# Optimization experiments

Hardware: AMD Instinct MI355X
Metric: run time of the kernel (lower is better)

The kernel has to match this reference:

```python
import jax, jax.numpy as jnp
import numpy as np

N_NODES = 50000
N_EDGES = 800000
H_DIM = 64
N_RELS = 8
N_BASES = 2
N_LAYERS = 2


def setup_inputs() -> dict:
    key = jax.random.key(0)
    ks = jax.random.split(key, 10)
    scale = 1.0 / np.sqrt(H_DIM)
    features = jax.random.normal(ks[0], (N_NODES, H_DIM), dtype=jnp.float32)
    src = jax.random.randint(ks[1], (N_EDGES,), 0, N_NODES, dtype=jnp.int32)
    dst = jax.random.randint(ks[2], (N_EDGES,), 0, N_NODES, dtype=jnp.int32)
    etype = jax.random.randint(ks[3], (N_EDGES,), 0, N_RELS, dtype=jnp.int32)
    # basis weights V: [L, B, H, H], coefficients comp: [L, R, B]
    V = jax.random.normal(ks[4], (N_LAYERS, N_BASES, H_DIM, H_DIM), dtype=jnp.float32) * scale
    comp = jax.random.normal(ks[5], (N_LAYERS, N_RELS, N_BASES), dtype=jnp.float32)
    loop_w = jax.random.normal(ks[6], (N_LAYERS, H_DIM, H_DIM), dtype=jnp.float32) * scale
    layer_bias = jnp.zeros((N_LAYERS, H_DIM), dtype=jnp.float32)
    fc_w = jax.random.normal(ks[7], (1, N_NODES * H_DIM), dtype=jnp.float32) * (1.0 / np.sqrt(N_NODES * H_DIM))
    fc_b = jnp.zeros((1,), dtype=jnp.float32)
    return {
        "features": features, "V": V, "comp": comp, "loop_w": loop_w,
        "layer_bias": layer_bias, "fc_w": fc_w, "fc_b": fc_b,
        "src": src, "dst": dst, "etype": etype,
    }


def reference(features, V, comp, loop_w, layer_bias, fc_w, fc_b, src, dst, etype):
    N, H = features.shape
    L = V.shape[0]
    x = features
    for l in range(L):
        # basis decomposition: project nodes through each basis first (N*B*H, cheap),
        # then mix per-edge with relation coefficients -> avoids per-edge [H,H] weights
        proj = jnp.einsum('ni,bio->nbo', x, V[l])          # [N, B, H]
        msg = jnp.einsum('eb,ebo->eo', comp[l][etype], proj[src])  # [E, H]
        agg = jax.ops.segment_sum(msg, dst, num_segments=N)        # [N, H]
        h = agg + x @ loop_w[l] + layer_bias[l]
        x = jax.nn.relu(h) if l < L - 1 else h
    flat = x.reshape(1, -1)                                # [1, N*H]
    return jax.nn.sigmoid(flat @ fc_w.T + fc_b)            # [1, 1]
```

## Files before the change

kernel.cpp:

```cpp
#include <hip/hip_runtime.h>
#include <hip/hip_bf16.h>
#include <math.h>

#define N_NODES 50000
#define N_EDGES 800000
#define HDIM 64

#define NBUCKET 392
#define BSHIFT  7
#define NLOC    128
#define BCAP    3072

typedef short bf16x8 __attribute__((ext_vector_type(8)));
typedef float f32x4  __attribute__((ext_vector_type(4)));
typedef unsigned short ushort_t;

__device__ __forceinline__ ushort_t f2bf(float f) {
    __hip_bfloat16 b = __float2bfloat16(f);
    return *(ushort_t*)&b;
}

__global__ __launch_bounds__(256) void prep_kernel(
    const float* __restrict__ features, ushort_t* __restrict__ x_bf,
    const float* __restrict__ V, const float* __restrict__ lw,
    ushort_t* __restrict__ Wt, int* __restrict__ bucketFill,
    float* __restrict__ scalar, int* __restrict__ done)
{
    const int b = blockIdx.x;
    const int t = threadIdx.x;
    if (b < 3125) {
        const int i = b * 256 + t;
        const float4 v = ((const float4*)features)[i];
        ushort4 o = { f2bf(v.x), f2bf(v.y), f2bf(v.z), f2bf(v.w) };
        *(ushort4*)&x_bf[(size_t)i * 4] = o;
    } else if (b < 3221) {
        const int e = (b - 3125) * 256 + t;
        const int l = e / 12288, r = e % 12288;
        const int n = r / 192, k = r % 192;
        const int sel = k >> 6, i = k & 63;
        const float val = (sel < 2) ? V[l * 8192 + sel * 4096 + i * 64 + n]
                                    : lw[l * 4096 + i * 64 + n];
        Wt[e] = f2bf(val);
    } else {
        for (int i = t; i < NBUCKET; i += 256) bucketFill[i] = 0;
        if (t == 0) { scalar[0] = 0.0f; done[0] = 0; }
    }
}

__global__ __launch_bounds__(256) void bucket_scatter(
    const int* __restrict__ src, const int* __restrict__ dst,
    const int* __restrict__ etype, int* __restrict__ bucketFill,
    unsigned int* __restrict__ buf)
{
    __shared__ int cnt[NBUCKET];
    __shared__ int base[NBUCKET];
    const int t = threadIdx.x;
    for (int i = t; i < NBUCKET; i += 256) cnt[i] = 0;
    __syncthreads();

    int rank[8], bkt[8];
    unsigned pay[8];
    bool valid[8];
#pragma unroll
    for (int k = 0; k < 8; ++k) {
        const int e = blockIdx.x * 2048 + k * 256 + t;
        valid[k] = (e < N_EDGES);
        if (valid[k]) {
            const int d = dst[e];
            const int b = d >> BSHIFT;
            bkt[k] = b;
            pay[k] = (unsigned)src[e] | ((unsigned)etype[e] << 16)
                   | ((unsigned)(d & (NLOC - 1)) << 19);
            rank[k] = atomicAdd(&cnt[b], 1);
        }
    }
    __syncthreads();
    for (int i = t; i < NBUCKET; i += 256)
        base[i] = atomicAdd(&bucketFill[i], cnt[i]);
    __syncthreads();
#pragma unroll
    for (int k = 0; k < 8; ++k) {
        if (valid[k]) {
            const int pos = base[bkt[k]] + rank[k];
            if (pos < BCAP) buf[bkt[k] * BCAP + pos] = pay[k];
        }
    }
}

__global__ __launch_bounds__(256) void bucket_sort(
    const unsigned int* __restrict__ buf, const int* __restrict__ bucketFill,
    unsigned int* __restrict__ edges, int* __restrict__ row_ptr)
{
    __shared__ int hist[NLOC];
    __shared__ int lscan[NLOC];
    __shared__ int cnt2[NLOC];
    __shared__ int sraw[448];
    __shared__ int sexc[448];
    const int b = blockIdx.x;
    const int t = threadIdx.x;

    if (t < NLOC) { hist[t] = 0; cnt2[t] = 0; }
    for (int i = t; i < 448; i += 256)
        sraw[i] = (i < NBUCKET) ? bucketFill[i] : 0;
    __syncthreads();

    if (t < 64) {
        int carry = 0;
        for (int c = 0; c < 7; ++c) {
            const int h = sraw[c * 64 + t];
            int x = h;
#pragma unroll
            for (int off = 1; off < 64; off <<= 1) {
                int u = __shfl_up(x, off, 64);
                if (t >= off) x += u;
            }
            sexc[c * 64 + t] = carry + x - h;
            carry += __shfl(x, 63, 64);
        }
    }
    __syncthreads();
    const int cntb = min(sraw[b], BCAP);
    const int bb   = sexc[b];

    for (int i0 = t; i0 < cntb; i0 += 1024) {
        const bool v1 = i0 + 256 < cntb, v2 = i0 + 512 < cntb, v3 = i0 + 768 < cntb;
        const unsigned p0 = buf[b * BCAP + i0];
        unsigned p1 = 0, p2 = 0, p3 = 0;
        if (v1) p1 = buf[b * BCAP + i0 + 256];
        if (v2) p2 = buf[b * BCAP + i0 + 512];
        if (v3) p3 = buf[b * BCAP + i0 + 768];
        atomicAdd(&hist[p0 >> 19], 1);
        if (v1) atomicAdd(&hist[p1 >> 19], 1);
        if (v2) atomicAdd(&hist[p2 >> 19], 1);
        if (v3) atomicAdd(&hist[p3 >> 19], 1);
    }
    __syncthreads();

    if (t < 64) {
        int carry = 0;
        for (int c = 0; c < 2; ++c) {
            const int h = hist[c * 64 + t];
            int x = h;
#pragma unroll
            for (int off = 1; off < 64; off <<= 1) {
                int u = __shfl_up(x, off, 64);
                if (t >= off) x += u;
            }
            lscan[c * 64 + t] = carry + x - h;
            carry += __shfl(x, 63, 64);
        }
    }
    __syncthreads();

    const int n0 = b << BSHIFT;
    if (t < NLOC) {
        const int g = n0 + t;
        if (g < N_NODES) row_ptr[g] = bb + lscan[t];
    }
    if (b == NBUCKET - 1 && t == 0) row_ptr[N_NODES] = bb + cntb;

    for (int i0 = t; i0 < cntb; i0 += 1024) {
        const bool v1 = i0 + 256 < cntb, v2 = i0 + 512 < cntb, v3 = i0 + 768 < cntb;
        const unsigned p0 = buf[b * BCAP + i0];
        unsigned p1 = 0, p2 = 0, p3 = 0;
        if (v1) p1 = buf[b * BCAP + i0 + 256];
        if (v2) p2 = buf[b * BCAP + i0 + 512];
        if (v3) p3 = buf[b * BCAP + i0 + 768];
        {
            const int d = p0 >> 19;
            const int r = atomicAdd(&cnt2[d], 1);
            edges[bb + lscan[d] + r] = p0;
        }
        if (v1) { const int d = p1 >> 19; const int r = atomicAdd(&cnt2[d], 1);
                  edges[bb + lscan[d] + r] = p1; }
        if (v2) { const int d = p2 >> 19; const int r = atomicAdd(&cnt2[d], 1);
                  edges[bb + lscan[d] + r] = p2; }
        if (v3) { const int d = p3 >> 19; const int r = atomicAdd(&cnt2[d], 1);
                  edges[bb + lscan[d] + r] = p3; }
    }
}

__global__ __launch_bounds__(256) void aggregate_v4(
    const ushort_t* __restrict__ x,
    const unsigned int* __restrict__ edges,
    const int* __restrict__ row_ptr,
    const float* __restrict__ comp_l,
    ushort_t* __restrict__ y)
{
    __shared__ float scomp[16];
    const int t = threadIdx.x;
    if (t < 16) scomp[t] = comp_l[t];
    __syncthreads();

    const int lane = t & 63;
    const int wv   = t >> 6;
    const int g    = lane >> 4;
    const int fq   = lane & 15;
    const int n    = blockIdx.x * 16 + wv * 4 + g;

    const int beg = row_ptr[n];
    const int end = row_ptr[n + 1];

    float a0[4], a1[4];
#pragma unroll
    for (int i = 0; i < 4; ++i) { a0[i] = 0.f; a1[i] = 0.f; }

    for (int j = beg; j < end; j += 4) {
        unsigned p[4];
#pragma unroll
        for (int k = 0; k < 4; ++k) {
            const int e = j + k;
            p[k] = edges[(e < end) ? e : (end - 1)];
        }
        uint2 u[4];
#pragma unroll
        for (int k = 0; k < 4; ++k)
            u[k] = *(const uint2*)&x[(size_t)(p[k] & 0xFFFFu) * 64 + fq * 4];
        float2 c[4];
#pragma unroll
        for (int k = 0; k < 4; ++k) {
            c[k] = *(const float2*)&scomp[((p[k] >> 16) & 7u) * 2];
            if (j + k >= end) { c[k].x = 0.f; c[k].y = 0.f; }
        }
#pragma unroll
        for (int k = 0; k < 4; ++k) {
            const float f0 = __uint_as_float(u[k].x << 16);
            const float f1 = __uint_as_float(u[k].x & 0xFFFF0000u);
            const float f2 = __uint_as_float(u[k].y << 16);
            const float f3 = __uint_as_float(u[k].y & 0xFFFF0000u);
            a0[0] = fmaf(c[k].x, f0, a0[0]); a1[0] = fmaf(c[k].y, f0, a1[0]);
            a0[1] = fmaf(c[k].x, f1, a0[1]); a1[1] = fmaf(c[k].y, f1, a1[1]);
            a0[2] = fmaf(c[k].x, f2, a0[2]); a1[2] = fmaf(c[k].y, f2, a1[2]);
            a0[3] = fmaf(c[k].x, f3, a0[3]); a1[3] = fmaf(c[k].y, f3, a1[3]);
        }
    }

    ushort4 s0 = { f2bf(a0[0]), f2bf(a0[1]), f2bf(a0[2]), f2bf(a0[3]) };
    ushort4 s1 = { f2bf(a1[0]), f2bf(a1[1]), f2bf(a1[2]), f2bf(a1[3]) };
    *(ushort4*)&y[(size_t)n * 128 + fq * 4]      = s0;
    *(ushort4*)&y[(size_t)n * 128 + 64 + fq * 4] = s1;
}

template <bool FUSE>
__global__ __launch_bounds__(256) void mfma_transform(
    const ushort_t* __restrict__ y_bf,
    const ushort_t* __restrict__ x_bf,
    const ushort_t* __restrict__ Wt,
    const float* __restrict__ bias,
    const float* __restrict__ fcw,
    ushort_t* __restrict__ xout,
    float* __restrict__ scalar,
    const float* __restrict__ fcb,
    int* __restrict__ done,
    float* __restrict__ outp)
{
    __shared__ __align__(16) ushort_t su[64 * 200];
    __shared__ float sred[4];
    const int t = threadIdx.x;
    const int w = t >> 6;
    const int lane = t & 63;
    const int c16 = lane & 15;
    const int quad = lane >> 4;
    const int tile = blockIdx.x;

    bf16x8 wf[6];
#pragma unroll
    for (int kf = 0; kf < 6; ++kf)
        wf[kf] = *(const bf16x8*)&Wt[(w * 16 + c16) * 192 + kf * 32 + quad * 8];
    const float bv = bias[w * 16 + c16];

#pragma unroll
    for (int k = 0; k < 6; ++k) {
        const int cid = t + 256 * k;
        const int row = cid / 24;
        const int part = cid % 24;
        const int n = tile * 64 + row;
        uint4 v = {0u, 0u, 0u, 0u};
        if (n < N_NODES) {
            v = (part < 16) ? *(const uint4*)&y_bf[(size_t)n * 128 + part * 8]
                            : *(const uint4*)&x_bf[(size_t)n * 64 + (part - 16) * 8];
        }
        *(uint4*)&su[row * 200 + part * 8] = v;
    }
    __syncthreads();

    float fsum = 0.f;
#pragma unroll
    for (int mt = 0; mt < 4; ++mt) {
        f32x4 acc = {bv, bv, bv, bv};
#pragma unroll
        for (int kf = 0; kf < 6; ++kf) {
            const bf16x8 af =
                *(const bf16x8*)&su[(mt * 16 + c16) * 200 + kf * 32 + quad * 8];
            acc = __builtin_amdgcn_mfma_f32_16x16x32_bf16(af, wf[kf], acc, 0, 0, 0);
        }
        const int nodeb = tile * 64 + mt * 16 + quad * 4;
        if (FUSE) {
#pragma unroll
            for (int r = 0; r < 4; ++r) {
                const int n = nodeb + r;
                if (n < N_NODES)
                    fsum += acc[r] * fcw[(size_t)n * 64 + w * 16 + c16];
            }
        } else {
#pragma unroll
            for (int r = 0; r < 4; ++r) {
                const int n = nodeb + r;
                if (n < N_NODES)
                    xout[(size_t)n * 64 + w * 16 + c16] = f2bf(fmaxf(acc[r], 0.f));
            }
        }
    }

    if (FUSE) {
#pragma unroll
        for (int off = 32; off; off >>= 1) fsum += __shfl_down(fsum, off, 64);
        if (lane == 0) sred[w] = fsum;
        __syncthreads();
        if (t == 0) {
            atomicAdd(scalar, sred[0] + sred[1] + sred[2] + sred[3]);
            __threadfence();
            const int ticket = atomicAdd(done, 1);
            if (ticket == (int)gridDim.x - 1) {
                const float v = atomicAdd(scalar, 0.0f) + fcb[0];
                outp[0] = 1.0f / (1.0f + expf(-v));
            }
        }
    }
}

extern "C" void kernel_launch(void* const* d_in, const int* in_sizes, int n_in,
                              void* d_out, int out_size, void* d_ws, size_t ws_size,
                              hipStream_t stream)
{
    const float* features = (const float*)d_in[0];
    const float* V        = (const float*)d_in[1];
    const float* comp     = (const float*)d_in[2];
    const float* loop_w   = (const float*)d_in[3];
    const float* bias     = (const float*)d_in[4];
    const float* fc_w     = (const float*)d_in[5];
    const float* fc_b     = (const float*)d_in[6];
    const int*   src      = (const int*)d_in[7];
    const int*   dst      = (const int*)d_in[8];
    const int*   etype    = (const int*)d_in[9];
    float* out = (float*)d_out;

    char* ws = (char*)d_ws;
    ushort_t*     y_bf    = (ushort_t*)(ws);
    ushort_t*     x_bf    = (ushort_t*)(ws + 12800000);
    ushort_t*     x1_bf   = (ushort_t*)(ws + 19200000);
    ushort_t*     Wt      = (ushort_t*)(ws + 25600000);
    float*        scalar  = (float*)   (ws + 25649152);
    int*          done    = (int*)     (ws + 25649156);
    int*          bucketFill = (int*)  (ws + 25649280);
    int*          row_ptr = (int*)     (ws + 25650944);
    unsigned int* edges   = (unsigned int*)(ws + 25851008);
    unsigned int* buf     = (unsigned int*)(ws + 29051008);

    const int aggBlocks = N_NODES / 16;
    const int mtBlocks  = (N_NODES + 63) / 64;
    const int k1Blocks  = (N_EDGES + 2047) / 2048;

    prep_kernel<<<3222, 256, 0, stream>>>(features, x_bf, V, loop_w, Wt,
                                          bucketFill, scalar, done);
    bucket_scatter<<<k1Blocks, 256, 0, stream>>>(src, dst, etype, bucketFill, buf);
    bucket_sort<<<NBUCKET, 256, 0, stream>>>(buf, bucketFill, edges, row_ptr);

    aggregate_v4<<<aggBlocks, 256, 0, stream>>>(x_bf, edges, row_ptr, comp, y_bf);
    mfma_transform<false><<<mtBlocks, 256, 0, stream>>>(
        y_bf, x_bf, Wt, bias, nullptr, x1_bf, nullptr, nullptr, nullptr, nullptr);

    aggregate_v4<<<aggBlocks, 256, 0, stream>>>(x1_bf, edges, row_ptr, comp + 16, y_bf);
    mfma_transform<true><<<mtBlocks, 256, 0, stream>>>(
        y_bf, x1_bf, Wt + 12288, bias + 64, fc_w, nullptr, scalar, fc_b, done, out);
}
```

Measured before the change: 188.8 us.

## Gather FP8 node features in aggregation and fuse prep with edge bucketing

Node features are also written as FP8 e4m3 copies, which the aggregation kernels gather instead of bf16, halving the bytes per random row gather. Edge indices are now prefetched one iteration ahead in the aggregation loop. The prep and bucket-scatter kernels are merged into one launch, and the counter zeroing moves to a memset. The cost is extra FP8 writes and lower precision in the aggregated messages, which could matter for accuracy.

```diff
diff --git a/kernel.cpp b/kernel.cpp
--- a/kernel.cpp
+++ b/kernel.cpp
@@ -1,5 +1,6 @@
 #include <hip/hip_runtime.h>
 #include <hip/hip_bf16.h>
+#include <hip/hip_fp8.h>
 #include <math.h>
 
 #define N_NODES 50000
@@ -14,26 +15,69 @@
 typedef short bf16x8 __attribute__((ext_vector_type(8)));
 typedef float f32x4  __attribute__((ext_vector_type(4)));
 typedef unsigned short ushort_t;
+typedef unsigned char uchar_t;
 
 __device__ __forceinline__ ushort_t f2bf(float f) {
     __hip_bfloat16 b = __float2bfloat16(f);
     return *(ushort_t*)&b;
 }
 
-__global__ __launch_bounds__(256) void prep_kernel(
+__device__ __forceinline__ unsigned pk_fp8x4(float a, float b, float c, float d) {
+#if __has_builtin(__builtin_amdgcn_cvt_pk_fp8_f32)
+    int r = __builtin_amdgcn_cvt_pk_fp8_f32(a, b, 0, false);
+    r = __builtin_amdgcn_cvt_pk_fp8_f32(c, d, r, true);
+    return (unsigned)r;
+#else
+    __hip_fp8_e4m3 fa(a), fb(b), fc(c), fd(d);
+    return (unsigned)fa.__x | ((unsigned)fb.__x << 8)
+         | ((unsigned)fc.__x << 16) | ((unsigned)fd.__x << 24);
+#endif
+}
+__device__ __forceinline__ uchar_t f2fp8(float a) {
+#if __has_builtin(__builtin_amdgcn_cvt_pk_fp8_f32)
+    return (uchar_t)(__builtin_amdgcn_cvt_pk_fp8_f32(a, 0.f, 0, false) & 0xFF);
+#else
+    __hip_fp8_e4m3 fa(a);
+    return (uchar_t)fa.__x;
+#endif
+}
+__device__ __forceinline__ void fp8x4_to_f32(unsigned u, float* f) {
+#if __has_builtin(__builtin_amdgcn_cvt_f32_fp8)
+    f[0] = __builtin_amdgcn_cvt_f32_fp8(u, 0);
+    f[1] = __builtin_amdgcn_cvt_f32_fp8(u, 1);
+    f[2] = __builtin_amdgcn_cvt_f32_fp8(u, 2);
+    f[3] = __builtin_amdgcn_cvt_f32_fp8(u, 3);
+#else
+    __hip_fp8_e4m3 v0, v1, v2, v3;
+    v0.__x = (uchar_t)(u);       v1.__x = (uchar_t)(u >> 8);
+    v2.__x = (uchar_t)(u >> 16); v3.__x = (uchar_t)(u >> 24);
+    f[0] = (float)v0; f[1] = (float)v1; f[2] = (float)v2; f[3] = (float)v3;
+#endif
+}
+
+__global__ __launch_bounds__(256) void prep_scatter(
     const float* __restrict__ features, ushort_t* __restrict__ x_bf,
+    uchar_t* __restrict__ x8,
     const float* __restrict__ V, const float* __restrict__ lw,
-    ushort_t* __restrict__ Wt, int* __restrict__ bucketFill,
-    float* __restrict__ scalar, int* __restrict__ done)
+    ushort_t* __restrict__ Wt,
+    const int* __restrict__ src, const int* __restrict__ dst,
+    const int* __restrict__ etype, int* __restrict__ bucketFill,
+    unsigned int* __restrict__ buf)
 {
+    __shared__ int cnt[NBUCKET];
+    __shared__ int base[NBUCKET];
     const int b = blockIdx.x;
     const int t = threadIdx.x;
+
     if (b < 3125) {
         const int i = b * 256 + t;
         const float4 v = ((const float4*)features)[i];
         ushort4 o = { f2bf(v.x), f2bf(v.y), f2bf(v.z), f2bf(v.w) };
         *(ushort4*)&x_bf[(size_t)i * 4] = o;
-    } else if (b < 3221) {
+        ((unsigned*)x8)[i] = pk_fp8x4(v.x, v.y, v.z, v.w);
+        return;
+    }
+    if (b < 3221) {
         const int e = (b - 3125) * 256 + t;
         const int l = e / 12288, r = e % 12288;
         const int n = r / 192, k = r % 192;
@@ -41,20 +85,10 @@
         const float val = (sel < 2) ? V[l * 8192 + sel * 4096 + i * 64 + n]
                                     : lw[l * 4096 + i * 64 + n];
         Wt[e] = f2bf(val);
-    } else {
-        for (int i = t; i < NBUCKET; i += 256) bucketFill[i] = 0;
-        if (t == 0) { scalar[0] = 0.0f; done[0] = 0; }
-    }
-}
-
-__global__ __launch_bounds__(256) void bucket_scatter(
-    const int* __restrict__ src, const int* __restrict__ dst,
-    const int* __restrict__ etype, int* __restrict__ bucketFill,
-    unsigned int* __restrict__ buf)
-{
-    __shared__ int cnt[NBUCKET];
-    __shared__ int base[NBUCKET];
-    const int t = threadIdx.x;
+        return;
+    }
+
+    const int sb = b - 3221;
     for (int i = t; i < NBUCKET; i += 256) cnt[i] = 0;
     __syncthreads();
 
@@ -63,15 +97,15 @@
     bool valid[8];
 #pragma unroll
     for (int k = 0; k < 8; ++k) {
-        const int e = blockIdx.x * 2048 + k * 256 + t;
+        const int e = sb * 2048 + k * 256 + t;
         valid[k] = (e < N_EDGES);
         if (valid[k]) {
             const int d = dst[e];
-            const int b = d >> BSHIFT;
-            bkt[k] = b;
+            const int bk = d >> BSHIFT;
+            bkt[k] = bk;
             pay[k] = (unsigned)src[e] | ((unsigned)etype[e] << 16)
                    | ((unsigned)(d & (NLOC - 1)) << 19);
-            rank[k] = atomicAdd(&cnt[b], 1);
+            rank[k] = atomicAdd(&cnt[bk], 1);
         }
     }
     __syncthreads();
@@ -180,8 +214,8 @@
     }
 }
 
-__global__ __launch_bounds__(256) void aggregate_v4(
-    const ushort_t* __restrict__ x,
+__global__ __launch_bounds__(256) void aggregate_v6(
+    const uchar_t* __restrict__ x8,
     const unsigned int* __restrict__ edges,
     const int* __restrict__ row_ptr,
     const float* __restrict__ comp_l,
@@ -205,33 +239,36 @@
 #pragma unroll
     for (int i = 0; i < 4; ++i) { a0[i] = 0.f; a1[i] = 0.f; }
 
-    for (int j = beg; j < end; j += 4) {
-        unsigned p[4];
-#pragma unroll
-        for (int k = 0; k < 4; ++k) {
-            const int e = j + k;
-            p[k] = edges[(e < end) ? e : (end - 1)];
-        }
-        uint2 u[4];
-#pragma unroll
-        for (int k = 0; k < 4; ++k)
-            u[k] = *(const uint2*)&x[(size_t)(p[k] & 0xFFFFu) * 64 + fq * 4];
-        float2 c[4];
-#pragma unroll
-        for (int k = 0; k < 4; ++k) {
-            c[k] = *(const float2*)&scomp[((p[k] >> 16) & 7u) * 2];
-            if (j + k >= end) { c[k].x = 0.f; c[k].y = 0.f; }
-        }
-#pragma unroll
-        for (int k = 0; k < 4; ++k) {
-            const float f0 = __uint_as_float(u[k].x << 16);
-            const float f1 = __uint_as_float(u[k].x & 0xFFFF0000u);
-            const float f2 = __uint_as_float(u[k].y << 16);
-            const float f3 = __uint_as_float(u[k].y & 0xFFFF0000u);
-            a0[0] = fmaf(c[k].x, f0, a0[0]); a1[0] = fmaf(c[k].y, f0, a1[0]);
-            a0[1] = fmaf(c[k].x, f1, a0[1]); a1[1] = fmaf(c[k].y, f1, a1[1]);
-            a0[2] = fmaf(c[k].x, f2, a0[2]); a1[2] = fmaf(c[k].y, f2, a1[2]);
-            a0[3] = fmaf(c[k].x, f3, a0[3]); a1[3] = fmaf(c[k].y, f3, a1[3]);
+    if (beg < end) {
+        unsigned pc[4];
+#pragma unroll
+        for (int k = 0; k < 4; ++k) pc[k] = edges[min(beg + k, end - 1)];
+
+        for (int j = beg; j < end; j += 4) {
+            unsigned u[4];
+#pragma unroll
+            for (int k = 0; k < 4; ++k)
+                u[k] = *(const unsigned*)&x8[(size_t)(pc[k] & 0xFFFFu) * 64 + fq * 4];
+            unsigned pn[4];
+#pragma unroll
+            for (int k = 0; k < 4; ++k) pn[k] = edges[min(j + 4 + k, end - 1)];
+            float2 c[4];
+#pragma unroll
+            for (int k = 0; k < 4; ++k) {
+                c[k] = *(const float2*)&scomp[((pc[k] >> 16) & 7u) * 2];
+                if (j + k >= end) { c[k].x = 0.f; c[k].y = 0.f; }
+            }
+#pragma unroll
+            for (int k = 0; k < 4; ++k) {
+                float f[4];
+                fp8x4_to_f32(u[k], f);
+                a0[0] = fmaf(c[k].x, f[0], a0[0]); a1[0] = fmaf(c[k].y, f[0], a1[0]);
+                a0[1] = fmaf(c[k].x, f[1], a0[1]); a1[1] = fmaf(c[k].y, f[1], a1[1]);
+                a0[2] = fmaf(c[k].x, f[2], a0[2]); a1[2] = fmaf(c[k].y, f[2], a1[2]);
+                a0[3] = fmaf(c[k].x, f[3], a0[3]); a1[3] = fmaf(c[k].y, f[3], a1[3]);
+            }
+#pragma unroll
+            for (int k = 0; k < 4; ++k) pc[k] = pn[k];
         }
     }
 
@@ -249,6 +286,7 @@
     const float* __restrict__ bias,
     const float* __restrict__ fcw,
     ushort_t* __restrict__ xout,
+    uchar_t* __restrict__ xout8,
     float* __restrict__ scalar,
     const float* __restrict__ fcb,
     int* __restrict__ done,
@@ -306,8 +344,11 @@
 #pragma unroll
             for (int r = 0; r < 4; ++r) {
                 const int n = nodeb + r;
-                if (n < N_NODES)
-                    xout[(size_t)n * 64 + w * 16 + c16] = f2bf(fmaxf(acc[r], 0.f));
+                if (n < N_NODES) {
+                    const float rl = fmaxf(acc[r], 0.f);
+                    xout[(size_t)n * 64 + w * 16 + c16]  = f2bf(rl);
+                    xout8[(size_t)n * 64 + w * 16 + c16] = f2fp8(rl);
+                }
             }
         }
     }
@@ -349,28 +390,31 @@
     ushort_t*     y_bf    = (ushort_t*)(ws);
     ushort_t*     x_bf    = (ushort_t*)(ws + 12800000);
     ushort_t*     x1_bf   = (ushort_t*)(ws + 19200000);
-    ushort_t*     Wt      = (ushort_t*)(ws + 25600000);
-    float*        scalar  = (float*)   (ws + 25649152);
-    int*          done    = (int*)     (ws + 25649156);
-    int*          bucketFill = (int*)  (ws + 25649280);
-    int*          row_ptr = (int*)     (ws + 25650944);
-    unsigned int* edges   = (unsigned int*)(ws + 25851008);
-    unsigned int* buf     = (unsigned int*)(ws + 29051008);
+    uchar_t*      x8      = (uchar_t*) (ws + 25600000);
+    uchar_t*      x1_8    = (uchar_t*) (ws + 28800000);
+    ushort_t*     Wt      = (ushort_t*)(ws + 32000000);
+    float*        scalar  = (float*)   (ws + 32049152);
+    int*          done    = (int*)     (ws + 32049156);
+    int*          bucketFill = (int*)  (ws + 32049160);
+    int*          row_ptr = (int*)     (ws + 32051072);
+    unsigned int* edges   = (unsigned int*)(ws + 32251264);
+    unsigned int* buf     = (unsigned int*)(ws + 35451264);
 
     const int aggBlocks = N_NODES / 16;
     const int mtBlocks  = (N_NODES + 63) / 64;
-    const int k1Blocks  = (N_EDGES + 2047) / 2048;
-
-    prep_kernel<<<3222, 256, 0, stream>>>(features, x_bf, V, loop_w, Wt,
-                                          bucketFill, scalar, done);
-    bucket_scatter<<<k1Blocks, 256, 0, stream>>>(src, dst, etype, bucketFill, buf);
+    const int psBlocks  = 3221 + 391;
+
+    hipMemsetAsync(scalar, 0, 1576, stream);
+    prep_scatter<<<psBlocks, 256, 0, stream>>>(features, x_bf, x8, V, loop_w, Wt,
+                                               src, dst, etype, bucketFill, buf);
     bucket_sort<<<NBUCKET, 256, 0, stream>>>(buf, bucketFill, edges, row_ptr);
 
-    aggregate_v4<<<aggBlocks, 256, 0, stream>>>(x_bf, edges, row_ptr, comp, y_bf);
+    aggregate_v6<<<aggBlocks, 256, 0, stream>>>(x8, edges, row_ptr, comp, y_bf);
     mfma_transform<false><<<mtBlocks, 256, 0, stream>>>(
-        y_bf, x_bf, Wt, bias, nullptr, x1_bf, nullptr, nullptr, nullptr, nullptr);
-
-    aggregate_v4<<<aggBlocks, 256, 0, stream>>>(x1_bf, edges, row_ptr, comp + 16, y_bf);
+        y_bf, x_bf, Wt, bias, nullptr, x1_bf, x1_8, nullptr, nullptr, nullptr, nullptr);
+
+    aggregate_v6<<<aggBlocks, 256, 0, stream>>>(x1_8, edges, row_ptr, comp + 16, y_bf);
     mfma_transform<true><<<mtBlocks, 256, 0, stream>>>(
-        y_bf, x1_bf, Wt + 12288, bias + 64, fc_w, nullptr, scalar, fc_b, done, out);
-}
+        y_bf, x1_bf, Wt + 12288, bias + 64, fc_w, nullptr, nullptr,
+        scalar, fc_b, done, out);
+}
```

New measurement: 193.4 us. 2.4% more time.

## Sort nodes by degree within buckets to balance aggregation wavefronts

Applied to the files above, without the earlier changes.

The bucket sort now also counting-sorts the 128 nodes of each bucket by in-degree and writes a permutation array. The aggregation kernel walks nodes in that order, so the four nodes sharing a wavefront have similar edge counts and less time is lost to divergent loop trip counts. Padding slots beyond N_NODES are skipped. The cost is an extra indirection load per node, scattered output writes, and a small amount of extra work in the sort kernel.

```diff
diff --git a/kernel.cpp b/kernel.cpp
--- a/kernel.cpp
+++ b/kernel.cpp
@@ -10,6 +10,7 @@
 #define BSHIFT  7
 #define NLOC    128
 #define BCAP    3072
+#define NVIRT   (NBUCKET * NLOC)
 
 typedef short bf16x8 __attribute__((ext_vector_type(8)));
 typedef float f32x4  __attribute__((ext_vector_type(4)));
@@ -89,13 +90,15 @@
 
 __global__ __launch_bounds__(256) void bucket_sort(
     const unsigned int* __restrict__ buf, const int* __restrict__ bucketFill,
-    unsigned int* __restrict__ edges, int* __restrict__ row_ptr)
+    unsigned int* __restrict__ edges, int* __restrict__ row_ptr,
+    int* __restrict__ perm)
 {
     __shared__ int hist[NLOC];
     __shared__ int lscan[NLOC];
     __shared__ int cnt2[NLOC];
     __shared__ int sraw[448];
     __shared__ int sexc[448];
+    __shared__ int dh[64];
     const int b = blockIdx.x;
     const int t = threadIdx.x;
 
@@ -159,6 +162,27 @@
     }
     if (b == NBUCKET - 1 && t == 0) row_ptr[N_NODES] = bb + cntb;
 
+    if (t < 64) dh[t] = 0;
+    __syncthreads();
+    if (t < NLOC) atomicAdd(&dh[min(hist[t], 63)], 1);
+    __syncthreads();
+    if (t < 64) {
+        const int h = dh[t];
+        int x = h;
+#pragma unroll
+        for (int off = 1; off < 64; off <<= 1) {
+            int u = __shfl_up(x, off, 64);
+            if (t >= off) x += u;
+        }
+        dh[t] = x - h;
+    }
+    __syncthreads();
+    if (t < NLOC) {
+        const int dr  = min(hist[t], 63);
+        const int pos = atomicAdd(&dh[dr], 1);
+        perm[n0 + pos] = n0 + t;
+    }
+
     for (int i0 = t; i0 < cntb; i0 += 1024) {
         const bool v1 = i0 + 256 < cntb, v2 = i0 + 512 < cntb, v3 = i0 + 768 < cntb;
         const unsigned p0 = buf[b * BCAP + i0];
@@ -180,10 +204,11 @@
     }
 }
 
-__global__ __launch_bounds__(256) void aggregate_v4(
+__global__ __launch_bounds__(256) void aggregate_v7(
     const ushort_t* __restrict__ x,
     const unsigned int* __restrict__ edges,
     const int* __restrict__ row_ptr,
+    const int* __restrict__ perm,
     const float* __restrict__ comp_l,
     ushort_t* __restrict__ y)
 {
@@ -196,10 +221,11 @@
     const int wv   = t >> 6;
     const int g    = lane >> 4;
     const int fq   = lane & 15;
-    const int n    = blockIdx.x * 16 + wv * 4 + g;
-
-    const int beg = row_ptr[n];
-    const int end = row_ptr[n + 1];
+    const int vi   = blockIdx.x * 16 + wv * 4 + g;
+    const int n    = perm[vi];
+
+    int beg = 0, end = 0;
+    if (n < N_NODES) { beg = row_ptr[n]; end = row_ptr[n + 1]; }
 
     float a0[4], a1[4];
 #pragma unroll
@@ -235,10 +261,12 @@
         }
     }
 
-    ushort4 s0 = { f2bf(a0[0]), f2bf(a0[1]), f2bf(a0[2]), f2bf(a0[3]) };
-    ushort4 s1 = { f2bf(a1[0]), f2bf(a1[1]), f2bf(a1[2]), f2bf(a1[3]) };
-    *(ushort4*)&y[(size_t)n * 128 + fq * 4]      = s0;
-    *(ushort4*)&y[(size_t)n * 128 + 64 + fq * 4] = s1;
+    if (n < N_NODES) {
+        ushort4 s0 = { f2bf(a0[0]), f2bf(a0[1]), f2bf(a0[2]), f2bf(a0[3]) };
+        ushort4 s1 = { f2bf(a1[0]), f2bf(a1[1]), f2bf(a1[2]), f2bf(a1[3]) };
+        *(ushort4*)&y[(size_t)n * 128 + fq * 4]      = s0;
+        *(ushort4*)&y[(size_t)n * 128 + 64 + fq * 4] = s1;
+    }
 }
 
 template <bool FUSE>
@@ -356,21 +384,24 @@
     int*          row_ptr = (int*)     (ws + 25650944);
     unsigned int* edges   = (unsigned int*)(ws + 25851008);
     unsigned int* buf     = (unsigned int*)(ws + 29051008);
-
-    const int aggBlocks = N_NODES / 16;
+    int*          perm    = (int*)     (ws + 33867904);
+
+    const int aggBlocks = NVIRT / 16;
     const int mtBlocks  = (N_NODES + 63) / 64;
     const int k1Blocks  = (N_EDGES + 2047) / 2048;
 
     prep_kernel<<<3222, 256, 0, stream>>>(features, x_bf, V, loop_w, Wt,
                                           bucketFill, scalar, done);
     bucket_scatter<<<k1Blocks, 256, 0, stream>>>(src, dst, etype, bucketFill, buf);
-    bucket_sort<<<NBUCKET, 256, 0, stream>>>(buf, bucketFill, edges, row_ptr);
-
-    aggregate_v4<<<aggBlocks, 256, 0, stream>>>(x_bf, edges, row_ptr, comp, y_bf);
+    bucket_sort<<<NBUCKET, 256, 0, stream>>>(buf, bucketFill, edges, row_ptr, perm);
+
+    aggregate_v7<<<aggBlocks, 256, 0, stream>>>(x_bf, edges, row_ptr, perm,
+                                                comp, y_bf);
     mfma_transform<false><<<mtBlocks, 256, 0, stream>>>(
         y_bf, x_bf, Wt, bias, nullptr, x1_bf, nullptr, nullptr, nullptr, nullptr);
 
-    aggregate_v4<<<aggBlocks, 256, 0, stream>>>(x1_bf, edges, row_ptr, comp + 16, y_bf);
+    aggregate_v7<<<aggBlocks, 256, 0, stream>>>(x1_bf, edges, row_ptr, perm,
+                                                comp + 16, y_bf);
     mfma_transform<true><<<mtBlocks, 256, 0, stream>>>(
         y_bf, x1_bf, Wt + 12288, bias + 64, fc_w, nullptr, scalar, fc_b, done, out);
 }
```

After: 193.4 us. 1.02x slower.

## Fuse edge bucket scatter into prep kernel and halve bucket size

Applied to the files above, without the earlier changes.

Merges the bucket scatter into the prep kernel and zeroes the counters, scalar and done flag with a hipMemsetAsync, removing one kernel launch. Buckets shrink from 128 to 64 nodes (784 buckets, capacity 1280), which doubles the number of sort blocks and lets the local scan run as a single wavefront pass. The smaller capacity raises the risk of silently dropping edges if a bucket overflows, and the global bucket scan now has more chunks to walk.

```diff
diff --git a/kernel.cpp b/kernel.cpp
--- a/kernel.cpp
+++ b/kernel.cpp
@@ -6,10 +6,11 @@
 #define N_EDGES 800000
 #define HDIM 64
 
-#define NBUCKET 392
-#define BSHIFT  7
-#define NLOC    128
-#define BCAP    3072
+#define NBUCKET 784
+#define BSHIFT  6
+#define NLOC    64
+#define BCAP    1280
+#define NBPAD   832
 
 typedef short bf16x8 __attribute__((ext_vector_type(8)));
 typedef float f32x4  __attribute__((ext_vector_type(4)));
@@ -20,70 +21,67 @@
     return *(ushort_t*)&b;
 }
 
-__global__ __launch_bounds__(256) void prep_kernel(
+__global__ __launch_bounds__(256) void prep_scatter(
     const float* __restrict__ features, ushort_t* __restrict__ x_bf,
     const float* __restrict__ V, const float* __restrict__ lw,
-    ushort_t* __restrict__ Wt, int* __restrict__ bucketFill,
-    float* __restrict__ scalar, int* __restrict__ done)
-{
+    ushort_t* __restrict__ Wt,
+    const int* __restrict__ src, const int* __restrict__ dst,
+    const int* __restrict__ etype, int* __restrict__ bucketFill,
+    unsigned int* __restrict__ buf)
+{
+    __shared__ int cnt[NBUCKET];
+    __shared__ int base[NBUCKET];
     const int b = blockIdx.x;
     const int t = threadIdx.x;
-    if (b < 3125) {
-        const int i = b * 256 + t;
+
+    if (b < 391) {
+        for (int i = t; i < NBUCKET; i += 256) cnt[i] = 0;
+        __syncthreads();
+
+        int rank[8], bkt[8];
+        unsigned pay[8];
+        bool valid[8];
+#pragma unroll
+        for (int k = 0; k < 8; ++k) {
+            const int e = b * 2048 + k * 256 + t;
+            valid[k] = (e < N_EDGES);
+            if (valid[k]) {
+                const int d = dst[e];
+                const int bk = d >> BSHIFT;
+                bkt[k] = bk;
+                pay[k] = (unsigned)src[e] | ((unsigned)etype[e] << 16)
+                       | ((unsigned)(d & (NLOC - 1)) << 19);
+                rank[k] = atomicAdd(&cnt[bk], 1);
+            }
+        }
+        __syncthreads();
+        for (int i = t; i < NBUCKET; i += 256)
+            base[i] = atomicAdd(&bucketFill[i], cnt[i]);
+        __syncthreads();
+#pragma unroll
+        for (int k = 0; k < 8; ++k) {
+            if (valid[k]) {
+                const int pos = base[bkt[k]] + rank[k];
+                if (pos < BCAP) buf[bkt[k] * BCAP + pos] = pay[k];
+            }
+        }
+        return;
+    }
+    if (b < 3516) {
+        const int i = (b - 391) * 256 + t;
         const float4 v = ((const float4*)features)[i];
         ushort4 o = { f2bf(v.x), f2bf(v.y), f2bf(v.z), f2bf(v.w) };
         *(ushort4*)&x_bf[(size_t)i * 4] = o;
-    } else if (b < 3221) {
-        const int e = (b - 3125) * 256 + t;
+        return;
+    }
+    {
+        const int e = (b - 3516) * 256 + t;
         const int l = e / 12288, r = e % 12288;
         const int n = r / 192, k = r % 192;
         const int sel = k >> 6, i = k & 63;
         const float val = (sel < 2) ? V[l * 8192 + sel * 4096 + i * 64 + n]
                                     : lw[l * 4096 + i * 64 + n];
         Wt[e] = f2bf(val);
-    } else {
-        for (int i = t; i < NBUCKET; i += 256) bucketFill[i] = 0;
-        if (t == 0) { scalar[0] = 0.0f; done[0] = 0; }
-    }
-}
-
-__global__ __launch_bounds__(256) void bucket_scatter(
-    const int* __restrict__ src, const int* __restrict__ dst,
-    const int* __restrict__ etype, int* __restrict__ bucketFill,
-    unsigned int* __restrict__ buf)
-{
-    __shared__ int cnt[NBUCKET];
-    __shared__ int base[NBUCKET];
-    const int t = threadIdx.x;
-    for (int i = t; i < NBUCKET; i += 256) cnt[i] = 0;
-    __syncthreads();
-
-    int rank[8], bkt[8];
-    unsigned pay[8];
-    bool valid[8];
-#pragma unroll
-    for (int k = 0; k < 8; ++k) {
-        const int e = blockIdx.x * 2048 + k * 256 + t;
-        valid[k] = (e < N_EDGES);
-        if (valid[k]) {
-            const int d = dst[e];
-            const int b = d >> BSHIFT;
-            bkt[k] = b;
-            pay[k] = (unsigned)src[e] | ((unsigned)etype[e] << 16)
-                   | ((unsigned)(d & (NLOC - 1)) << 19);
-            rank[k] = atomicAdd(&cnt[b], 1);
-        }
-    }
-    __syncthreads();
-    for (int i = t; i < NBUCKET; i += 256)
-        base[i] = atomicAdd(&bucketFill[i], cnt[i]);
-    __syncthreads();
-#pragma unroll
-    for (int k = 0; k < 8; ++k) {
-        if (valid[k]) {
-            const int pos = base[bkt[k]] + rank[k];
-            if (pos < BCAP) buf[bkt[k] * BCAP + pos] = pay[k];
-        }
     }
 }
 
@@ -94,19 +92,19 @@
     __shared__ int hist[NLOC];
     __shared__ int lscan[NLOC];
     __shared__ int cnt2[NLOC];
-    __shared__ int sraw[448];
-    __shared__ int sexc[448];
+    __shared__ int sraw[NBPAD];
+    __shared__ int sexc[NBPAD];
     const int b = blockIdx.x;
     const int t = threadIdx.x;
 
     if (t < NLOC) { hist[t] = 0; cnt2[t] = 0; }
-    for (int i = t; i < 448; i += 256)
+    for (int i = t; i < NBPAD; i += 256)
         sraw[i] = (i < NBUCKET) ? bucketFill[i] : 0;
     __syncthreads();
 
     if (t < 64) {
         int carry = 0;
-        for (int c = 0; c < 7; ++c) {
+        for (int c = 0; c < 13; ++c) {
             const int h = sraw[c * 64 + t];
             int x = h;
 #pragma unroll
@@ -137,18 +135,14 @@
     __syncthreads();
 
     if (t < 64) {
-        int carry = 0;
-        for (int c = 0; c < 2; ++c) {
-            const int h = hist[c * 64 + t];
-            int x = h;
-#pragma unroll
-            for (int off = 1; off < 64; off <<= 1) {
-                int u = __shfl_up(x, off, 64);
-                if (t >= off) x += u;
-            }
-            lscan[c * 64 + t] = carry + x - h;
-            carry += __shfl(x, 63, 64);
-        }
+        const int h = hist[t];
+        int x = h;
+#pragma unroll
+        for (int off = 1; off < 64; off <<= 1) {
+            int u = __shfl_up(x, off, 64);
+            if (t >= off) x += u;
+        }
+        lscan[t] = x - h;
     }
     __syncthreads();
 
@@ -352,18 +346,18 @@
     ushort_t*     Wt      = (ushort_t*)(ws + 25600000);
     float*        scalar  = (float*)   (ws + 25649152);
     int*          done    = (int*)     (ws + 25649156);
-    int*          bucketFill = (int*)  (ws + 25649280);
-    int*          row_ptr = (int*)     (ws + 25650944);
-    unsigned int* edges   = (unsigned int*)(ws + 25851008);
-    unsigned int* buf     = (unsigned int*)(ws + 29051008);
+    int*          bucketFill = (int*)  (ws + 25649160);
+    int*          row_ptr = (int*)     (ws + 25652352);
+    unsigned int* edges   = (unsigned int*)(ws + 25852416);
+    unsigned int* buf     = (unsigned int*)(ws + 29052416);
 
     const int aggBlocks = N_NODES / 16;
     const int mtBlocks  = (N_NODES + 63) / 64;
-    const int k1Blocks  = (N_EDGES + 2047) / 2048;
-
-    prep_kernel<<<3222, 256, 0, stream>>>(features, x_bf, V, loop_w, Wt,
-                                          bucketFill, scalar, done);
-    bucket_scatter<<<k1Blocks, 256, 0, stream>>>(src, dst, etype, bucketFill, buf);
+    const int psBlocks  = 391 + 3125 + 96;
+
+    hipMemsetAsync(scalar, 0, 3144, stream);
+    prep_scatter<<<psBlocks, 256, 0, stream>>>(features, x_bf, V, loop_w, Wt,
+                                               src, dst, etype, bucketFill, buf);
     bucket_sort<<<NBUCKET, 256, 0, stream>>>(buf, bucketFill, edges, row_ptr);
 
     aggregate_v4<<<aggBlocks, 256, 0, stream>>>(x_bf, edges, row_ptr, comp, y_bf);
```

New measurement: 198.5 us. +5.1%, slower.
